# Kernel tuning notes

Hardware: AMD Instinct MI355X
Metric: run time of the kernel (lower is better)

The kernel has to match this reference:

```python
import jax, jax.numpy as jnp
import numpy as np

N_NODES = 50000
N_EDGES = 1200000
F_IN = 128
F_EDGE = 32
H = 78


def _p(key, shape, fan_in):
    return jax.random.normal(key, shape, dtype=jnp.float32) / np.sqrt(fan_in)


def setup_inputs() -> dict:
    key = jax.random.key(0)
    ks = jax.random.split(key, 20)
    x = jax.random.normal(ks[0], (N_NODES, F_IN), dtype=jnp.float32)
    edge_index = jax.random.randint(ks[1], (2, N_EDGES), 0, N_NODES, dtype=jnp.int32)
    edge_attr = jax.random.normal(ks[2], (N_EDGES, F_EDGE), dtype=jnp.float32)
    return {
        "x": x, "edge_index": edge_index, "edge_attr": edge_attr,
        # GATConv layer 1
        "W1": _p(ks[3], (F_IN, H), F_IN), "as1": _p(ks[4], (H,), H), "ad1": _p(ks[5], (H,), H),
        "b1": jnp.zeros((H,), jnp.float32),
        # GATConv layer 2
        "W2": _p(ks[6], (H, H), H), "as2": _p(ks[7], (H,), H), "ad2": _p(ks[8], (H,), H),
        "b2": jnp.zeros((H,), jnp.float32),
        # edge MLP
        "Wm1": _p(ks[9], (F_EDGE, H), F_EDGE), "bm1": jnp.zeros((H,), jnp.float32),
        "Wm2": _p(ks[10], (H, H), H), "bm2": jnp.zeros((H,), jnp.float32),
        # final edge head
        "Wf": _p(ks[11], (3 * H, 1), 3 * H), "bf": jnp.zeros((1,), jnp.float32),
    }


def _gat_conv(x, W, a_src, a_dst, bias, src, dst, n_nodes):
    """PyG GATConv, heads=1, negative_slope=0.2, self-loops already in src/dst."""
    h = x @ W                                   # [N, H]
    alpha_s = h @ a_src                         # [N]
    alpha_d = h @ a_dst                         # [N]
    e = jax.nn.leaky_relu(alpha_s[src] + alpha_d[dst], negative_slope=0.2)  # [E']
    # softmax over incoming edges per destination node
    m = jax.ops.segment_max(e, dst, num_segments=n_nodes)
    e = jnp.exp(e - m[dst])
    s = jax.ops.segment_sum(e, dst, num_segments=n_nodes)
    alpha = e / (s[dst] + 1e-16)                # [E']
    out = jax.ops.segment_sum(alpha[:, None] * h[src], dst, num_segments=n_nodes)
    return out + bias


def reference(x, edge_index, edge_attr, W1, as1, ad1, b1, W2, as2, ad2, b2,
              Wm1, bm1, Wm2, bm2, Wf, bf):
    n_nodes = x.shape[0]
    loop = jnp.arange(n_nodes, dtype=edge_index.dtype)
    src = jnp.concatenate([edge_index[0], loop])  # add self-loops (PyG default)
    dst = jnp.concatenate([edge_index[1], loop])

    h = _gat_conv(x, W1, as1, ad1, b1, src, dst, n_nodes)
    h = jax.nn.relu(h)  # dropout is identity in eval mode
    h = _gat_conv(h, W2, as2, ad2, b2, src, dst, n_nodes)

    ef = jax.nn.relu(edge_attr @ Wm1 + bm1) @ Wm2 + bm2            # [E, H]
    emb = jnp.concatenate([h[edge_index[0]], h[edge_index[1]], ef], axis=1)  # [E, 3H]
    return jnp.squeeze(emb @ Wf + bf, axis=-1)                     # [E]
```

## Files before the change

### kernel.cpp

```cpp
#include <hip/hip_runtime.h>
#include <math.h>

#define NN 50000
#define NE 1200000
#define FIN 128
#define FE 32
#define H 78
#define HP 80
#define ETOT (NE + NN)

#define NPB 64
#define NBUCK ((NN + NPB - 1) / NPB)
#define BCAP 2560

#define EB 3200
#define NBE ((ETOT + EB - 1) / EB)
#define GHN (NBUCK * NBE)
#define GS_NB ((GHN + 1023) / 1024)

#define GB ((NN + 63) / 64)
#define FE_WAVES 18750
#define FEB ((FE_WAVES + 3) / 4)

typedef __attribute__((ext_vector_type(8))) short bf16x8;
typedef __attribute__((ext_vector_type(4))) float f32x4;

__device__ __forceinline__ unsigned short f2bf(float f) {
  unsigned u = __float_as_uint(f);
  return (unsigned short)((u + 0x7FFFu + ((u >> 16) & 1u)) >> 16);
}
__device__ __forceinline__ float bf2f(unsigned short b) {
  return __uint_as_float((unsigned)b << 16);
}

union Frag { uint4 q; bf16x8 v; unsigned short u[8]; };

__device__ __forceinline__ void wperm_one(const float* __restrict__ W, int K, int idx,
                                          uint4* __restrict__ out) {
  int lane = idx & 63;
  int fid = idx >> 6;
  int split = fid & 1;
  int sg = fid >> 1;
  int step = sg / 5, g = sg % 5;
  int kg = lane >> 4, l15 = lane & 15;
  int col = g * 16 + l15;
  Frag f;
#pragma unroll
  for (int e = 0; e < 8; ++e) {
    int k = step * 32 + kg * 8 + e;
    float v = (k < K && col < H) ? W[(size_t)k * H + col] : 0.f;
    unsigned short h = f2bf(v);
    if (split) h = f2bf(v - bf2f(h));
    f.u[e] = h;
  }
  out[idx] = f.q;
}

__global__ void prep_all(const float* __restrict__ W1, const float* __restrict__ W2,
                         const float* __restrict__ Wm2, const float* __restrict__ bm2,
                         const float* __restrict__ Wf, const float* __restrict__ bf,
                         uint4* __restrict__ wperm1, uint4* __restrict__ wperm2,
                         float* __restrict__ wpc) {
  int b = blockIdx.x, t = threadIdx.x;
  if (b < 10) {
    wperm_one(W1, FIN, b * 256 + t, wperm1);
  } else if (b < 18) {
    int idx = (b - 10) * 256 + t;
    if (idx < 30 * 64) wperm_one(W2, H, idx, wperm2);
  } else {
    int k = t;
    if (k < H) {
      float s = 0.f;
      for (int j = 0; j < H; ++j) s += Wm2[k * H + j] * Wf[2 * H + j];
      wpc[k] = s;
    } else if (k == H) {
      float s = 0.f;
      for (int j = 0; j < H; ++j) s += bm2[j] * Wf[2 * H + j];
      wpc[H] = s + bf[0];
    }
  }
}

template<int STEPS, int LDA>
__device__ __forceinline__ void gemm_body(const float* __restrict__ A,
    const uint4* __restrict__ wperm, const float* __restrict__ as,
    const float* __restrict__ ad, unsigned* __restrict__ hb,
    float* __restrict__ asv, float* __restrict__ adv, int blk, int tid) {
  int lane = tid & 63;
  int gw = blk * 4 + (tid >> 6);
  int n0w = gw * 16;
  if (n0w >= NN) return;
  int l15 = lane & 15, kg = lane >> 4;
  f32x4 acc[5];
#pragma unroll
  for (int g = 0; g < 5; ++g) acc[g] = (f32x4){0.f, 0.f, 0.f, 0.f};

#pragma unroll
  for (int step = 0; step < STEPS; ++step) {
    int k0 = step * 32 + kg * 8;
    bf16x8 ah, al;
    if (k0 < LDA) {
      int row = n0w + l15;
      if (row >= NN) row = NN - 1;
      const float* ar = A + (size_t)row * LDA + k0;
      float4 f0 = *reinterpret_cast<const float4*>(ar);
      float4 f1 = *reinterpret_cast<const float4*>(ar + 4);
      float fv[8] = {f0.x, f0.y, f0.z, f0.w, f1.x, f1.y, f1.z, f1.w};
#pragma unroll
      for (int e = 0; e < 8; ++e) {
        unsigned short h = f2bf(fv[e]);
        ah[e] = (short)h;
        al[e] = (short)f2bf(fv[e] - bf2f(h));
      }
    } else {
#pragma unroll
      for (int e = 0; e < 8; ++e) { ah[e] = 0; al[e] = 0; }
    }
#pragma unroll
    for (int g = 0; g < 5; ++g) {
      Frag wh, wl;
      wh.q = wperm[((size_t)(step * 5 + g) * 2 + 0) * 64 + lane];
      wl.q = wperm[((size_t)(step * 5 + g) * 2 + 1) * 64 + lane];
      acc[g] = __builtin_amdgcn_mfma_f32_16x16x32_bf16(ah, wh.v, acc[g], 0, 0, 0);
      acc[g] = __builtin_amdgcn_mfma_f32_16x16x32_bf16(al, wh.v, acc[g], 0, 0, 0);
      acc[g] = __builtin_amdgcn_mfma_f32_16x16x32_bf16(ah, wl.v, acc[g], 0, 0, 0);
    }
  }

  float asl[5], adl[5];
#pragma unroll
  for (int g = 0; g < 5; ++g) {
    int col = g * 16 + l15;
    asl[g] = (col < H) ? as[col] : 0.f;
    adl[g] = (col < H) ? ad[col] : 0.f;
  }

#pragma unroll
  for (int r = 0; r < 4; ++r) {
    int node = n0w + kg * 4 + r;
#pragma unroll
    for (int g = 0; g < 5; ++g) {
      float c = acc[g][r];
      float cn = __shfl_xor(c, 1);
      if (!(l15 & 1) && node < NN)
        hb[(size_t)node * (HP / 2) + g * 8 + (l15 >> 1)] =
            (unsigned)f2bf(c) | ((unsigned)f2bf(cn) << 16);
    }
    float sa = 0.f, sd = 0.f;
#pragma unroll
    for (int g = 0; g < 5; ++g) {
      sa = fmaf(acc[g][r], asl[g], sa);
      sd = fmaf(acc[g][r], adl[g], sd);
    }
#pragma unroll
    for (int mask = 1; mask < 16; mask <<= 1) {
      sa += __shfl_xor(sa, mask);
      sd += __shfl_xor(sd, mask);
    }
    if (l15 == 0 && node < NN) { asv[node] = sa; adv[node] = sd; }
  }
}

__device__ __forceinline__ void bin_hist_body(const int* __restrict__ ei,
                                              int* __restrict__ gh, int b, int t) {
  __shared__ int hist[NBUCK];
  for (int k = t; k < NBUCK; k += 256) hist[k] = 0;
  __syncthreads();
  int e0 = b * EB;
  int e1 = min(e0 + EB, ETOT);
  for (int i = e0 + t; i < e1; i += 256) {
    int dst = (i < NE) ? ei[NE + i] : (i - NE);
    atomicAdd(&hist[dst >> 6], 1);
  }
  __syncthreads();
  for (int k = t; k < NBUCK; k += 256) gh[(size_t)k * NBE + b] = hist[k];
}

__device__ __forceinline__ void edge_mlp_body(const float* __restrict__ ea,
    const float* __restrict__ Wm1, const float* __restrict__ bm1,
    const float* __restrict__ wpc, float* __restrict__ es, int blk, int tid) {
  int lane = tid & 63;
  long gw = (long)blk * 4 + (tid >> 6);
  if (gw >= FE_WAVES) return;
  int l15 = lane & 15;
  int kg = lane >> 4;
  bf16x8 bfrag[5];
  float bm1c[5], wpcc[5];
#pragma unroll
  for (int g = 0; g < 5; ++g) {
    int col = g * 16 + l15;
    bool valid = col < H;
    bm1c[g] = valid ? bm1[col] : 0.f;
    wpcc[g] = valid ? wpc[col] : 0.f;
#pragma unroll
    for (int e = 0; e < 8; ++e) {
      int kk = kg * 8 + e;
      bfrag[g][e] = valid ? (short)f2bf(Wm1[kk * H + col]) : (short)0;
    }
  }
  float basec = wpc[H];
  int e0 = (int)(gw * 64);
#pragma unroll
  for (int t4 = 0; t4 < 4; ++t4) {
    int ebase = e0 + t4 * 16;
    const float* ar = ea + (size_t)(ebase + l15) * FE + kg * 8;
    float4 f0 = *reinterpret_cast<const float4*>(ar);
    float4 f1 = *reinterpret_cast<const float4*>(ar + 4);
    bf16x8 afrag;
    afrag[0] = (short)f2bf(f0.x); afrag[1] = (short)f2bf(f0.y);
    afrag[2] = (short)f2bf(f0.z); afrag[3] = (short)f2bf(f0.w);
    afrag[4] = (short)f2bf(f1.x); afrag[5] = (short)f2bf(f1.y);
    afrag[6] = (short)f2bf(f1.z); afrag[7] = (short)f2bf(f1.w);
    float es0 = 0.f, es1 = 0.f, es2 = 0.f, es3 = 0.f;
#pragma unroll
    for (int g = 0; g < 5; ++g) {
      f32x4 c = {0.f, 0.f, 0.f, 0.f};
      c = __builtin_amdgcn_mfma_f32_16x16x32_bf16(afrag, bfrag[g], c, 0, 0, 0);
      es0 = fmaf(fmaxf(c[0] + bm1c[g], 0.f), wpcc[g], es0);
      es1 = fmaf(fmaxf(c[1] + bm1c[g], 0.f), wpcc[g], es1);
      es2 = fmaf(fmaxf(c[2] + bm1c[g], 0.f), wpcc[g], es2);
      es3 = fmaf(fmaxf(c[3] + bm1c[g], 0.f), wpcc[g], es3);
    }
#pragma unroll
    for (int m = 1; m < 16; m <<= 1) {
      es0 += __shfl_xor(es0, m);
      es1 += __shfl_xor(es1, m);
      es2 += __shfl_xor(es2, m);
      es3 += __shfl_xor(es3, m);
    }
    if (l15 < 4) {
      float esv = (l15 == 0) ? es0 : (l15 == 1) ? es1 : (l15 == 2) ? es2 : es3;
      int e = ebase + kg * 4 + l15;
      es[e] = esv + basec;
    }
  }
}

__global__ __launch_bounds__(256)
void fuseA(const int* __restrict__ ei, int* __restrict__ gh,
           const float* __restrict__ x, const uint4* __restrict__ wperm1,
           const float* __restrict__ as1, const float* __restrict__ ad1,
           unsigned* __restrict__ hb, float* __restrict__ asv,
           float* __restrict__ adv,
           const float* __restrict__ ea, const float* __restrict__ Wm1,
           const float* __restrict__ bm1, const float* __restrict__ wpc,
           float* __restrict__ es) {
  int b = blockIdx.x, t = threadIdx.x;
  if (b < FEB) edge_mlp_body(ea, Wm1, bm1, wpc, es, b, t);
  else if (b < FEB + NBE) bin_hist_body(ei, gh, b - FEB, t);
  else gemm_body<4, FIN>(x, wperm1, as1, ad1, hb, asv, adv, b - FEB - NBE, t);
}

__global__ __launch_bounds__(256)
void gemm_mfma2(const float* __restrict__ A, const uint4* __restrict__ wperm,
                const float* __restrict__ as, const float* __restrict__ ad,
                unsigned* __restrict__ hb, float* __restrict__ asv,
                float* __restrict__ adv) {
  gemm_body<3, HP>(A, wperm, as, ad, hb, asv, adv, blockIdx.x, threadIdx.x);
}

__global__ void scan1g(const int* __restrict__ gh, int* __restrict__ gsum) {
  __shared__ int sh[256];
  int b = blockIdx.x, t = threadIdx.x;
  int i0 = b * 1024 + t * 4;
  int s = 0;
#pragma unroll
  for (int k = 0; k < 4; ++k) {
    int i = i0 + k;
    if (i < GHN) s += gh[i];
  }
  sh[t] = s;
  __syncthreads();
  for (int off = 128; off > 0; off >>= 1) {
    if (t < off) sh[t] += sh[t + off];
    __syncthreads();
  }
  if (t == 0) gsum[b] = sh[0];
}

__global__ void scan2g(const int* __restrict__ gsum, int* __restrict__ gboff) {
  __shared__ int sh[512];
  int t = threadIdx.x;
  sh[t] = (t < GS_NB) ? gsum[t] : 0;
  __syncthreads();
  for (int off = 1; off < 512; off <<= 1) {
    int v = (t >= off) ? sh[t - off] : 0;
    __syncthreads();
    sh[t] += v;
    __syncthreads();
  }
  if (t < GS_NB) gboff[t] = (t == 0) ? 0 : sh[t - 1];
}

__global__ void scan3g(const int* __restrict__ gh, const int* __restrict__ gboff,
                       int* __restrict__ goff) {
  __shared__ int sh[256];
  int b = blockIdx.x, t = threadIdx.x;
  int i0 = b * 1024 + t * 4;
  int v[4];
  int s = 0;
#pragma unroll
  for (int k = 0; k < 4; ++k) {
    int i = i0 + k;
    v[k] = (i < GHN) ? gh[i] : 0;
    s += v[k];
  }
  sh[t] = s;
  __syncthreads();
  for (int off = 1; off < 256; off <<= 1) {
    int u = (t >= off) ? sh[t - off] : 0;
    __syncthreads();
    sh[t] += u;
    __syncthreads();
  }
  int run = gboff[b] + ((t == 0) ? 0 : sh[t - 1]);
#pragma unroll
  for (int k = 0; k < 4; ++k) {
    int i = i0 + k;
    if (i < GHN) { goff[i] = run; run += v[k]; }
  }
}

__global__ __launch_bounds__(256)
void bin_place(const int* __restrict__ ei, const int* __restrict__ goff,
               unsigned* __restrict__ tmp) {
  __shared__ int cursor[NBUCK];
  int b = blockIdx.x, t = threadIdx.x;
  for (int k = t; k < NBUCK; k += 256) cursor[k] = goff[(size_t)k * NBE + b];
  __syncthreads();
  int e0 = b * EB;
  int e1 = min(e0 + EB, ETOT);
  for (int i = e0 + t; i < e1; i += 256) {
    int src, dst;
    if (i < NE) { src = ei[i]; dst = ei[NE + i]; }
    else { src = dst = i - NE; }
    int pos = atomicAdd(&cursor[dst >> 6], 1);
    tmp[pos] = ((unsigned)(dst & 63) << 17) | (unsigned)src;
  }
}

__global__ __launch_bounds__(256)
void bucket_build(const unsigned* __restrict__ tmp, const int* __restrict__ goff,
                  int* __restrict__ rowptr, int* __restrict__ srcs) {
  __shared__ int hist[NPB];
  __shared__ int offs[NPB];
  __shared__ int curs[NPB];
  __shared__ int srcs_l[BCAP];
  int b = blockIdx.x, t = threadIdx.x;
  int base = goff[(size_t)b * NBE];
  int next = (b + 1 < NBUCK) ? goff[(size_t)(b + 1) * NBE] : ETOT;
  int cnt = next - base;
  int n0 = b * NPB;
  if (t < NPB) hist[t] = 0;
  __syncthreads();
  for (int p = t; p < cnt; p += 256) {
    atomicAdd(&hist[tmp[base + p] >> 17], 1);
  }
  __syncthreads();
  if (t == 0) {
    int run = 0;
    for (int j = 0; j < NPB; ++j) { offs[j] = run; run += hist[j]; }
  }
  __syncthreads();
  if (t < NPB) {
    curs[t] = offs[t];
    int n = n0 + t;
    if (n < NN) rowptr[n] = base + offs[t];
  }
  if (b == NBUCK - 1 && t == 0) rowptr[NN] = ETOT;
  __syncthreads();
  for (int p = t; p < cnt; p += 256) {
    unsigned e = tmp[base + p];
    int dstoff = e >> 17;
    int src = (int)(e & 0x1FFFFu);
    int lp = atomicAdd(&curs[dstoff], 1);
    if (lp < BCAP) srcs_l[lp] = src;
    else srcs[base + lp] = src;
  }
  __syncthreads();
  int m = cnt < BCAP ? cnt : BCAP;
  for (int p = t; p < m; p += 256) srcs[base + p] = srcs_l[p];
}

template<int RELU, int FINAL>
__global__ __launch_bounds__(256)
void gat_fused(const int* __restrict__ rowptr, const int* __restrict__ srcs,
               const float* __restrict__ asv, const float* __restrict__ adv,
               const unsigned* __restrict__ hb, const float* __restrict__ bias,
               const float* __restrict__ Wf, float* __restrict__ outp,
               float* __restrict__ uu, float* __restrict__ vv) {
  int n = (blockIdx.x * 256 + threadIdx.x) >> 6;
  int lane = threadIdx.x & 63;
  if (n >= NN) return;
  int r0 = rowptr[n], r1 = rowptr[n + 1];
  int deg = r1 - r0;
  float advn = adv[n];

  int s0 = 0;
  float e0 = -INFINITY;
  if (lane < deg) {
    s0 = srcs[r0 + lane];
    float e = asv[s0] + advn;
    e0 = e > 0.f ? e : 0.2f * e;
  }
  float m = e0;
#pragma unroll
  for (int off = 1; off < 64; off <<= 1) m = fmaxf(m, __shfl_xor(m, off));
  float ssum = (lane < deg) ? __expf(e0 - m) : 0.f;
#pragma unroll
  for (int off = 1; off < 64; off <<= 1) ssum += __shfl_xor(ssum, off);
  for (int c = r0 + 64; c < r1; c += 64) {
    int p = c + lane;
    float e = -INFINITY;
    if (p < r1) {
      float t = asv[srcs[p]] + advn;
      e = t > 0.f ? t : 0.2f * t;
    }
    float cm = e;
#pragma unroll
    for (int off = 1; off < 64; off <<= 1) cm = fmaxf(cm, __shfl_xor(cm, off));
    float c2 = (p < r1) ? __expf(e - cm) : 0.f;
#pragma unroll
    for (int off = 1; off < 64; off <<= 1) c2 += __shfl_xor(c2, off);
    float mn = fmaxf(m, cm);
    ssum = ssum * __expf(m - mn) + c2 * __expf(cm - mn);
    m = mn;
  }
  float inv = 1.f / (ssum + 1e-16f);
  float alpha0 = (lane < deg) ? __expf(e0 - m) * inv : 0.f;

  int g6 = lane / 10;
  int lp = lane - g6 * 10;
  float4 aL = {0.f, 0.f, 0.f, 0.f}, aH = {0.f, 0.f, 0.f, 0.f};
  int nch = deg < 64 ? deg : 64;
  for (int base = 0; base < nch; base += 6) {
    int p = base + g6;
    bool act = (g6 < 6) && (p < nch);
    int idx = p < 63 ? p : 63;
    float al = __shfl(alpha0, idx);
    int s = __shfl(s0, idx);
    if (act) {
      uint4 q = *(reinterpret_cast<const uint4*>(hb + (size_t)s * (HP / 2)) + lp);
      aL.x = fmaf(al, bf2f((unsigned short)(q.x & 0xffff)), aL.x);
      aL.y = fmaf(al, bf2f((unsigned short)(q.x >> 16)), aL.y);
      aL.z = fmaf(al, bf2f((unsigned short)(q.y & 0xffff)), aL.z);
      aL.w = fmaf(al, bf2f((unsigned short)(q.y >> 16)), aL.w);
      aH.x = fmaf(al, bf2f((unsigned short)(q.z & 0xffff)), aH.x);
      aH.y = fmaf(al, bf2f((unsigned short)(q.z >> 16)), aH.y);
      aH.z = fmaf(al, bf2f((unsigned short)(q.w & 0xffff)), aH.z);
      aH.w = fmaf(al, bf2f((unsigned short)(q.w >> 16)), aH.w);
    }
  }
  for (int c = r0 + 64; c < r1; c += 64) {
    int p = c + lane;
    float al = 0.f;
    int s = 0;
    if (p < r1) {
      s = srcs[p];
      float t = asv[s] + advn;
      t = t > 0.f ? t : 0.2f * t;
      al = __expf(t - m) * inv;
    }
    int cnt = min(r1 - c, 64);
    for (int base = 0; base < cnt; base += 6) {
      int p2 = base + g6;
      bool act = (g6 < 6) && (p2 < cnt);
      int idx = p2 < 63 ? p2 : 63;
      float alq = __shfl(al, idx);
      int sq = __shfl(s, idx);
      if (act) {
        uint4 q = *(reinterpret_cast<const uint4*>(hb + (size_t)sq * (HP / 2)) + lp);
        aL.x = fmaf(alq, bf2f((unsigned short)(q.x & 0xffff)), aL.x);
        aL.y = fmaf(alq, bf2f((unsigned short)(q.x >> 16)), aL.y);
        aL.z = fmaf(alq, bf2f((unsigned short)(q.y & 0xffff)), aL.z);
        aL.w = fmaf(alq, bf2f((unsigned short)(q.y >> 16)), aL.w);
        aH.x = fmaf(alq, bf2f((unsigned short)(q.z & 0xffff)), aH.x);
        aH.y = fmaf(alq, bf2f((unsigned short)(q.z >> 16)), aH.y);
        aH.z = fmaf(alq, bf2f((unsigned short)(q.w & 0xffff)), aH.z);
        aH.w = fmaf(alq, bf2f((unsigned short)(q.w >> 16)), aH.w);
      }
    }
  }

  float o[8];
  float* av = reinterpret_cast<float*>(&aL);
#pragma unroll
  for (int j = 0; j < 4; ++j) {
    float v = av[j];
    o[j] = v + __shfl(v, lane + 10) + __shfl(v, lane + 20) + __shfl(v, lane + 30)
             + __shfl(v, lane + 40) + __shfl(v, lane + 50);
  }
  float* ah = reinterpret_cast<float*>(&aH);
#pragma unroll
  for (int j = 0; j < 4; ++j) {
    float v = ah[j];
    o[4 + j] = v + __shfl(v, lane + 10) + __shfl(v, lane + 20) + __shfl(v, lane + 30)
                 + __shfl(v, lane + 40) + __shfl(v, lane + 50);
  }

  if (FINAL) {
    float su = 0.f, sv = 0.f;
    if (lane < 10) {
      int c0 = lane * 8;
#pragma unroll
      for (int j = 0; j < 8; ++j) {
        int col = c0 + j;
        float oj = o[j] + ((col < H) ? bias[col] : 0.f);
        float wu = (col < H) ? Wf[col] : 0.f;
        float wv = (col < H) ? Wf[H + col] : 0.f;
        su = fmaf(oj, wu, su);
        sv = fmaf(oj, wv, sv);
      }
    }
#pragma unroll
    for (int off = 1; off < 64; off <<= 1) {
      su += __shfl_xor(su, off);
      sv += __shfl_xor(sv, off);
    }
    if (lane == 0) { uu[n] = su; vv[n] = sv; }
  } else {
    if (lane < 10) {
      int c0 = lane * 8;
      float4 w0, w1;
      float* pw = reinterpret_cast<float*>(&w0);
#pragma unroll
      for (int j = 0; j < 4; ++j) {
        int col = c0 + j;
        float oj = o[j] + ((col < H) ? bias[col] : 0.f);
        if (RELU) oj = fmaxf(oj, 0.f);
        pw[j] = (col < H) ? oj : 0.f;
      }
      float* pw1 = reinterpret_cast<float*>(&w1);
#pragma unroll
      for (int j = 0; j < 4; ++j) {
        int col = c0 + 4 + j;
        float oj = o[4 + j] + ((col < H) ? bias[col] : 0.f);
        if (RELU) oj = fmaxf(oj, 0.f);
        pw1[j] = (col < H) ? oj : 0.f;
      }
      float* orow = outp + (size_t)n * HP + c0;
      *reinterpret_cast<float4*>(orow) = w0;
      *reinterpret_cast<float4*>(orow + 4) = w1;
    }
  }
}

__global__ void final_out(const float* __restrict__ es, const int* __restrict__ ei,
                          const float* __restrict__ u, const float* __restrict__ v,
                          float* __restrict__ out) {
  int e = blockIdx.x * blockDim.x + threadIdx.x;
  if (e >= NE) return;
  out[e] = es[e] + u[ei[e]] + v[ei[NE + e]];
}

extern "C" void kernel_launch(void* const* d_in, const int* in_sizes, int n_in,
                              void* d_out, int out_size, void* d_ws, size_t ws_size,
                              hipStream_t stream) {
  const float* x   = (const float*)d_in[0];
  const int*   ei  = (const int*)d_in[1];
  const float* ea  = (const float*)d_in[2];
  const float* W1  = (const float*)d_in[3];
  const float* as1 = (const float*)d_in[4];
  const float* ad1 = (const float*)d_in[5];
  const float* b1  = (const float*)d_in[6];
  const float* W2  = (const float*)d_in[7];
  const float* as2 = (const float*)d_in[8];
  const float* ad2 = (const float*)d_in[9];
  const float* b2  = (const float*)d_in[10];
  const float* Wm1 = (const float*)d_in[11];
  const float* bm1 = (const float*)d_in[12];
  const float* Wm2 = (const float*)d_in[13];
  const float* bm2 = (const float*)d_in[14];
  const float* Wf  = (const float*)d_in[15];
  const float* bf  = (const float*)d_in[16];
  float* out = (float*)d_out;

  float* w = (float*)d_ws;
  float* bufB = w; w += (size_t)NN * HP;
  unsigned* hb = (unsigned*)w; w += (size_t)NN * (HP / 2);
  uint4* wperm1 = (uint4*)w; w += 4 * 40 * 64;
  uint4* wperm2 = (uint4*)w; w += 4 * 30 * 64;
  float* asv  = w; w += NN;
  float* adv  = w; w += NN;
  float* uu   = w; w += NN;
  float* vv   = w; w += NN;
  float* wpc  = w; w += HP;
  float* es   = w; w += NE;
  unsigned* tmp = (unsigned*)w; w += ETOT;
  int* rowptr = (int*)w; w += NN + 1;
  int* srcs   = (int*)w; w += ETOT;
  int* gh     = (int*)w; w += GHN;
  int* goff   = (int*)w; w += GHN;
  int* gsum   = (int*)w; w += GS_NB;
  int* gboff  = (int*)w; w += GS_NB;

  const int B = 256;
  dim3 gW((NN * 64 + B - 1) / B);
  dim3 gEo((NE + B - 1) / B);

  prep_all<<<19, B, 0, stream>>>(W1, W2, Wm2, bm2, Wf, bf, wperm1, wperm2, wpc);

  fuseA<<<FEB + NBE + GB, B, 0, stream>>>(ei, gh, x, wperm1, as1, ad1, hb, asv,
                                          adv, ea, Wm1, bm1, wpc, es);

  scan1g<<<GS_NB, B, 0, stream>>>(gh, gsum);
  scan2g<<<1, 512, 0, stream>>>(gsum, gboff);
  scan3g<<<GS_NB, B, 0, stream>>>(gh, gboff, goff);
  bin_place<<<NBE, B, 0, stream>>>(ei, goff, tmp);
  bucket_build<<<NBUCK, B, 0, stream>>>(tmp, goff, rowptr, srcs);

  gat_fused<1, 0><<<gW, B, 0, stream>>>(rowptr, srcs, asv, adv, hb, b1, Wf,
                                        bufB, uu, vv);

  gemm_mfma2<<<GB, B, 0, stream>>>(bufB, wperm2, as2, ad2, hb, asv, adv);
  gat_fused<0, 1><<<gW, B, 0, stream>>>(rowptr, srcs, asv, adv, hb, b2, Wf,
                                        nullptr, uu, vv);

  final_out<<<gEo, B, 0, stream>>>(es, ei, uu, vv, out);
}
```

Baseline: 221.4 us.

## Fuse edge MLP into final output kernel and split fused first-stage kernel

The edge-MLP computation moves from the combined first-stage kernel into the final output kernel. That kernel now computes the per-edge MLP score and adds u[src] and v[dst] directly, which removes the intermediate es buffer (1.2M floats written and read back). The old fused kernel that ran histogram, GEMM1 and edge MLP together is split back into separate bin_hist and templated gemm_mfma launches. The cost is an extra launch and the loss of concurrency between the edge MLP and the binning/GEMM work.

```diff
diff --git a/kernel.cpp b/kernel.cpp
--- a/kernel.cpp
+++ b/kernel.cpp
@@ -82,12 +82,14 @@
 }
 
 template<int STEPS, int LDA>
-__device__ __forceinline__ void gemm_body(const float* __restrict__ A,
-    const uint4* __restrict__ wperm, const float* __restrict__ as,
-    const float* __restrict__ ad, unsigned* __restrict__ hb,
-    float* __restrict__ asv, float* __restrict__ adv, int blk, int tid) {
+__global__ __launch_bounds__(256)
+void gemm_mfma(const float* __restrict__ A, const uint4* __restrict__ wperm,
+               const float* __restrict__ as, const float* __restrict__ ad,
+               unsigned* __restrict__ hb, float* __restrict__ asv,
+               float* __restrict__ adv) {
+  int tid = threadIdx.x;
   int lane = tid & 63;
-  int gw = blk * 4 + (tid >> 6);
+  int gw = blockIdx.x * 4 + (tid >> 6);
   int n0w = gw * 16;
   if (n0w >= NN) return;
   int l15 = lane & 15, kg = lane >> 4;
@@ -161,9 +163,10 @@
   }
 }
 
-__device__ __forceinline__ void bin_hist_body(const int* __restrict__ ei,
-                                              int* __restrict__ gh, int b, int t) {
+__global__ __launch_bounds__(256)
+void bin_hist(const int* __restrict__ ei, int* __restrict__ gh) {
   __shared__ int hist[NBUCK];
+  int b = blockIdx.x, t = threadIdx.x;
   for (int k = t; k < NBUCK; k += 256) hist[k] = 0;
   __syncthreads();
   int e0 = b * EB;
@@ -174,89 +177,6 @@
   }
   __syncthreads();
   for (int k = t; k < NBUCK; k += 256) gh[(size_t)k * NBE + b] = hist[k];
-}
-
-__device__ __forceinline__ void edge_mlp_body(const float* __restrict__ ea,
-    const float* __restrict__ Wm1, const float* __restrict__ bm1,
-    const float* __restrict__ wpc, float* __restrict__ es, int blk, int tid) {
-  int lane = tid & 63;
-  long gw = (long)blk * 4 + (tid >> 6);
-  if (gw >= FE_WAVES) return;
-  int l15 = lane & 15;
-  int kg = lane >> 4;
-  bf16x8 bfrag[5];
-  float bm1c[5], wpcc[5];
-#pragma unroll
-  for (int g = 0; g < 5; ++g) {
-    int col = g * 16 + l15;
-    bool valid = col < H;
-    bm1c[g] = valid ? bm1[col] : 0.f;
-    wpcc[g] = valid ? wpc[col] : 0.f;
-#pragma unroll
-    for (int e = 0; e < 8; ++e) {
-      int kk = kg * 8 + e;
-      bfrag[g][e] = valid ? (short)f2bf(Wm1[kk * H + col]) : (short)0;
-    }
-  }
-  float basec = wpc[H];
-  int e0 = (int)(gw * 64);
-#pragma unroll
-  for (int t4 = 0; t4 < 4; ++t4) {
-    int ebase = e0 + t4 * 16;
-    const float* ar = ea + (size_t)(ebase + l15) * FE + kg * 8;
-    float4 f0 = *reinterpret_cast<const float4*>(ar);
-    float4 f1 = *reinterpret_cast<const float4*>(ar + 4);
-    bf16x8 afrag;
-    afrag[0] = (short)f2bf(f0.x); afrag[1] = (short)f2bf(f0.y);
-    afrag[2] = (short)f2bf(f0.z); afrag[3] = (short)f2bf(f0.w);
-    afrag[4] = (short)f2bf(f1.x); afrag[5] = (short)f2bf(f1.y);
-    afrag[6] = (short)f2bf(f1.z); afrag[7] = (short)f2bf(f1.w);
-    float es0 = 0.f, es1 = 0.f, es2 = 0.f, es3 = 0.f;
-#pragma unroll
-    for (int g = 0; g < 5; ++g) {
-      f32x4 c = {0.f, 0.f, 0.f, 0.f};
-      c = __builtin_amdgcn_mfma_f32_16x16x32_bf16(afrag, bfrag[g], c, 0, 0, 0);
-      es0 = fmaf(fmaxf(c[0] + bm1c[g], 0.f), wpcc[g], es0);
-      es1 = fmaf(fmaxf(c[1] + bm1c[g], 0.f), wpcc[g], es1);
-      es2 = fmaf(fmaxf(c[2] + bm1c[g], 0.f), wpcc[g], es2);
-      es3 = fmaf(fmaxf(c[3] + bm1c[g], 0.f), wpcc[g], es3);
-    }
-#pragma unroll
-    for (int m = 1; m < 16; m <<= 1) {
-      es0 += __shfl_xor(es0, m);
-      es1 += __shfl_xor(es1, m);
-      es2 += __shfl_xor(es2, m);
-      es3 += __shfl_xor(es3, m);
-    }
-    if (l15 < 4) {
-      float esv = (l15 == 0) ? es0 : (l15 == 1) ? es1 : (l15 == 2) ? es2 : es3;
-      int e = ebase + kg * 4 + l15;
-      es[e] = esv + basec;
-    }
-  }
-}
-
-__global__ __launch_bounds__(256)
-void fuseA(const int* __restrict__ ei, int* __restrict__ gh,
-           const float* __restrict__ x, const uint4* __restrict__ wperm1,
-           const float* __restrict__ as1, const float* __restrict__ ad1,
-           unsigned* __restrict__ hb, float* __restrict__ asv,
-           float* __restrict__ adv,
-           const float* __restrict__ ea, const float* __restrict__ Wm1,
-           const float* __restrict__ bm1, const float* __restrict__ wpc,
-           float* __restrict__ es) {
-  int b = blockIdx.x, t = threadIdx.x;
-  if (b < FEB) edge_mlp_body(ea, Wm1, bm1, wpc, es, b, t);
-  else if (b < FEB + NBE) bin_hist_body(ei, gh, b - FEB, t);
-  else gemm_body<4, FIN>(x, wperm1, as1, ad1, hb, asv, adv, b - FEB - NBE, t);
-}
-
-__global__ __launch_bounds__(256)
-void gemm_mfma2(const float* __restrict__ A, const uint4* __restrict__ wperm,
-                const float* __restrict__ as, const float* __restrict__ ad,
-                unsigned* __restrict__ hb, float* __restrict__ asv,
-                float* __restrict__ adv) {
-  gemm_body<3, HP>(A, wperm, as, ad, hb, asv, adv, blockIdx.x, threadIdx.x);
 }
 
 __global__ void scan1g(const int* __restrict__ gh, int* __restrict__ gsum) {
@@ -545,12 +465,67 @@
   }
 }
 
-__global__ void final_out(const float* __restrict__ es, const int* __restrict__ ei,
-                          const float* __restrict__ u, const float* __restrict__ v,
-                          float* __restrict__ out) {
-  int e = blockIdx.x * blockDim.x + threadIdx.x;
-  if (e >= NE) return;
-  out[e] = es[e] + u[ei[e]] + v[ei[NE + e]];
+__global__ __launch_bounds__(256)
+void final_edge_mfma(const int* __restrict__ ei, const float* __restrict__ ea,
+                     const float* __restrict__ Wm1, const float* __restrict__ bm1,
+                     const float* __restrict__ wpc, const float* __restrict__ u,
+                     const float* __restrict__ v, float* __restrict__ out) {
+  int lane = threadIdx.x & 63;
+  long gw = (long)blockIdx.x * 4 + (threadIdx.x >> 6);
+  if (gw >= FE_WAVES) return;
+  int l15 = lane & 15;
+  int kg = lane >> 4;
+  bf16x8 bfrag[5];
+  float bm1c[5], wpcc[5];
+#pragma unroll
+  for (int g = 0; g < 5; ++g) {
+    int col = g * 16 + l15;
+    bool valid = col < H;
+    bm1c[g] = valid ? bm1[col] : 0.f;
+    wpcc[g] = valid ? wpc[col] : 0.f;
+#pragma unroll
+    for (int e = 0; e < 8; ++e) {
+      int kk = kg * 8 + e;
+      bfrag[g][e] = valid ? (short)f2bf(Wm1[kk * H + col]) : (short)0;
+    }
+  }
+  float basec = wpc[H];
+  int e0 = (int)(gw * 64);
+#pragma unroll
+  for (int t = 0; t < 4; ++t) {
+    int ebase = e0 + t * 16;
+    const float* ar = ea + (size_t)(ebase + l15) * FE + kg * 8;
+    float4 f0 = *reinterpret_cast<const float4*>(ar);
+    float4 f1 = *reinterpret_cast<const float4*>(ar + 4);
+    bf16x8 afrag;
+    afrag[0] = (short)f2bf(f0.x); afrag[1] = (short)f2bf(f0.y);
+    afrag[2] = (short)f2bf(f0.z); afrag[3] = (short)f2bf(f0.w);
+    afrag[4] = (short)f2bf(f1.x); afrag[5] = (short)f2bf(f1.y);
+    afrag[6] = (short)f2bf(f1.z); afrag[7] = (short)f2bf(f1.w);
+    float es0 = 0.f, es1 = 0.f, es2 = 0.f, es3 = 0.f;
+#pragma unroll
+    for (int g = 0; g < 5; ++g) {
+      f32x4 c = {0.f, 0.f, 0.f, 0.f};
+      c = __builtin_amdgcn_mfma_f32_16x16x32_bf16(afrag, bfrag[g], c, 0, 0, 0);
+      es0 = fmaf(fmaxf(c[0] + bm1c[g], 0.f), wpcc[g], es0);
+      es1 = fmaf(fmaxf(c[1] + bm1c[g], 0.f), wpcc[g], es1);
+      es2 = fmaf(fmaxf(c[2] + bm1c[g], 0.f), wpcc[g], es2);
+      es3 = fmaf(fmaxf(c[3] + bm1c[g], 0.f), wpcc[g], es3);
+    }
+#pragma unroll
+    for (int m = 1; m < 16; m <<= 1) {
+      es0 += __shfl_xor(es0, m);
+      es1 += __shfl_xor(es1, m);
+      es2 += __shfl_xor(es2, m);
+      es3 += __shfl_xor(es3, m);
+    }
+    if (l15 < 4) {
+      float es = (l15 == 0) ? es0 : (l15 == 1) ? es1 : (l15 == 2) ? es2 : es3;
+      int e = ebase + kg * 4 + l15;
+      int s = ei[e], d = ei[NE + e];
+      out[e] = es + u[s] + v[d] + basec;
+    }
+  }
 }
 
 extern "C" void kernel_launch(void* const* d_in, const int* in_sizes, int n_in,
@@ -585,7 +560,6 @@
   float* uu   = w; w += NN;
   float* vv   = w; w += NN;
   float* wpc  = w; w += HP;
-  float* es   = w; w += NE;
   unsigned* tmp = (unsigned*)w; w += ETOT;
   int* rowptr = (int*)w; w += NN + 1;
   int* srcs   = (int*)w; w += ETOT;
@@ -596,25 +570,23 @@
 
   const int B = 256;
   dim3 gW((NN * 64 + B - 1) / B);
-  dim3 gEo((NE + B - 1) / B);
 
   prep_all<<<19, B, 0, stream>>>(W1, W2, Wm2, bm2, Wf, bf, wperm1, wperm2, wpc);
 
-  fuseA<<<FEB + NBE + GB, B, 0, stream>>>(ei, gh, x, wperm1, as1, ad1, hb, asv,
-                                          adv, ea, Wm1, bm1, wpc, es);
-
+  bin_hist<<<NBE, B, 0, stream>>>(ei, gh);
   scan1g<<<GS_NB, B, 0, stream>>>(gh, gsum);
   scan2g<<<1, 512, 0, stream>>>(gsum, gboff);
   scan3g<<<GS_NB, B, 0, stream>>>(gh, gboff, goff);
   bin_place<<<NBE, B, 0, stream>>>(ei, goff, tmp);
   bucket_build<<<NBUCK, B, 0, stream>>>(tmp, goff, rowptr, srcs);
 
+  gemm_mfma<4, FIN><<<GB, B, 0, stream>>>(x, wperm1, as1, ad1, hb, asv, adv);
   gat_fused<1, 0><<<gW, B, 0, stream>>>(rowptr, srcs, asv, adv, hb, b1, Wf,
                                         bufB, uu, vv);
 
-  gemm_mfma2<<<GB, B, 0, stream>>>(bufB, wperm2, as2, ad2, hb, asv, adv);
+  gemm_mfma<3, HP><<<GB, B, 0, stream>>>(bufB, wperm2, as2, ad2, hb, asv, adv);
   gat_fused<0, 1><<<gW, B, 0, stream>>>(rowptr, srcs, asv, adv, hb, b2, Wf,
                                         nullptr, uu, vv);
 
-  final_out<<<gEo, B, 0, stream>>>(es, ei, uu, vv, out);
-}
+  final_edge_mfma<<<FEB, B, 0, stream>>>(ei, ea, Wm1, bm1, wpc, uu, vv, out);
+}
```

Result: slower. 226.5 us (+2.3%).
